# Kernel optimization log

Hardware: AMD Instinct MI355X
Metric: run time of the kernel (lower is better)

The kernel has to match this reference:

```python
import math
import jax, jax.numpy as jnp
import numpy as np

EMB_DIM = 1024
CFG_N_HEADS = 16
# Faithful to the torch module: n_heads collapses to 1 when config.n_heads < emb_dim
N_HEADS = CFG_N_HEADS if CFG_N_HEADS >= EMB_DIM else 1


def setup_inputs() -> dict:
    key = jax.random.key(0)
    ks = jax.random.split(key, 11)
    B, T, C = 4, 2048, EMB_DIM
    s = 1.0 / math.sqrt(C)
    return {
        "q": jax.random.normal(ks[0], (B, T, C), jnp.float32),
        "k": jax.random.normal(ks[1], (B, T, C), jnp.float32),
        "v": jax.random.normal(ks[2], (B, T, C), jnp.float32),
        "Wq": jax.random.normal(ks[3], (C, C), jnp.float32) * s,
        "bq": jax.random.normal(ks[4], (C,), jnp.float32) * s,
        "Wk": jax.random.normal(ks[5], (C, C), jnp.float32) * s,
        "bk": jax.random.normal(ks[6], (C,), jnp.float32) * s,
        "Wv": jax.random.normal(ks[7], (C, C), jnp.float32) * s,
        "bv": jax.random.normal(ks[8], (C,), jnp.float32) * s,
        "Wff": jax.random.normal(ks[9], (C, C), jnp.float32) * s,
        "bff": jax.random.normal(ks[10], (C,), jnp.float32) * s,
    }


def reference(q, k, v, Wq, bq, Wk, bk, Wv, bv, Wff, bff):
    B, T, C = q.shape
    H = N_HEADS
    D = C // H  # head dim (== C here since H degenerates to 1)
    # torch Linear: x @ W.T + b
    qp = (q @ Wq.T + bq).reshape(B, T, H, D).transpose(0, 2, 1, 3)  # [B,H,T,D]
    kp = (k @ Wk.T + bk).reshape(B, T, H, D).transpose(0, 2, 1, 3)
    vp = (v @ Wv.T + bv).reshape(B, T, H, D).transpose(0, 2, 1, 3)
    scale = 1.0 / math.sqrt(D)
    scores = jnp.einsum('bhqd,bhkd->bhqk', qp, kp) * scale  # [B,H,T,T]
    causal = jnp.tril(jnp.ones((T, T), dtype=bool))
    scores = jnp.where(causal[None, None, :, :], scores, -jnp.inf)
    attn = jax.nn.softmax(scores, axis=-1)
    out = jnp.einsum('bhqk,bhkd->bhqd', attn, vp)  # [B,H,T,D]
    out = out.transpose(0, 2, 1, 3).reshape(B, T, C)
    return out @ Wff.T + bff
```

## Files before the change

### kernel.cpp

```cpp
#include <hip/hip_runtime.h>
#include <stdint.h>

typedef unsigned short u16;
typedef short v8s __attribute__((ext_vector_type(8)));
typedef float v4f __attribute__((ext_vector_type(4)));

#define BM 128
#define BN 128
#define BK 64

__device__ __forceinline__ float b2f(u16 b) {
  union { unsigned u; float f; } x; x.u = ((unsigned)b) << 16; return x.f;
}
__device__ __forceinline__ u16 f2b(float f) {
  union { float f; unsigned u; } x; x.f = f;
  unsigned r = x.u + 0x7fffu + ((x.u >> 16) & 1u);
  return (u16)(r >> 16);
}

__device__ __forceinline__ void async_copy16(const void* g, void* lds) {
  __builtin_amdgcn_global_load_lds(
      (const __attribute__((address_space(1))) void*)g,
      (__attribute__((address_space(3))) void*)(uint32_t)(uintptr_t)lds,
      16, 0, 0);
}

__device__ __forceinline__ void xcd_swz(int& bx, int& by) {
  const int gx = gridDim.x;
  const int nwg = gx * gridDim.y;
  const int ord = blockIdx.y * gx + blockIdx.x;
  const int q = nwg >> 3, r = nwg & 7;
  const int xcd = ord & 7, local = ord >> 3;
  const int base = xcd < r ? xcd * (q + 1) : r * (q + 1) + (xcd - r) * q;
  const int s = base + local;
  bx = s % gx;
  by = s / gx;
}

__device__ __forceinline__ void causal_pair_swz(int& bx, int& by) {
  const int gx = gridDim.x;
  const int ord = blockIdx.y * gx + blockIdx.x;
  const int k = ord & 7;
  const int j = ord >> 3;
  by = (j < gx) ? k : 15 - k;
  bx = (j < gx) ? j : j - gx;
}

__global__ __launch_bounds__(256) void cvt3_kernel(
    const float* __restrict__ i0, const float* __restrict__ i1,
    const float* __restrict__ i2, u16* __restrict__ o0, u16* __restrict__ o1,
    u16* __restrict__ o2, int n) {
  const int z = blockIdx.y;
  const float* in = z == 0 ? i0 : (z == 1 ? i1 : i2);
  u16* out = z == 0 ? o0 : (z == 1 ? o1 : o2);
  const int i = (blockIdx.x * 256 + threadIdx.x) * 8;
  if (i >= n) return;
  v4f a = *(const v4f*)(in + i);
  v4f b = *(const v4f*)(in + i + 4);
  v8s o;
#pragma unroll
  for (int j = 0; j < 4; j++) o[j] = (short)f2b(a[j]);
#pragma unroll
  for (int j = 0; j < 4; j++) o[4 + j] = (short)f2b(b[j]);
  *(v8s*)(out + i) = o;
}

__global__ __launch_bounds__(256) void cvt4_kernel(
    const float* __restrict__ i0, const float* __restrict__ i1,
    const float* __restrict__ i2, const float* __restrict__ i3,
    u16* __restrict__ o0, u16* __restrict__ o1, u16* __restrict__ o2,
    u16* __restrict__ o3, int n) {
  const int z = blockIdx.y;
  const float* in = z == 0 ? i0 : (z == 1 ? i1 : (z == 2 ? i2 : i3));
  u16* out = z == 0 ? o0 : (z == 1 ? o1 : (z == 2 ? o2 : o3));
  const int i = (blockIdx.x * 256 + threadIdx.x) * 8;
  if (i >= n) return;
  v4f a = *(const v4f*)(in + i);
  v4f b = *(const v4f*)(in + i + 4);
  v8s o;
#pragma unroll
  for (int j = 0; j < 4; j++) o[j] = (short)f2b(a[j]);
#pragma unroll
  for (int j = 0; j < 4; j++) o[4 + j] = (short)f2b(b[j]);
  *(v8s*)(out + i) = o;
}

template <bool HAS_BIAS, bool CAUSAL_K, bool OUT_F32>
__device__ __forceinline__ void gemm_body(
    const u16* __restrict__ A, int lda, const u16* __restrict__ Bm, int ldb,
    void* __restrict__ Cout_, int ldc, long cbase,
    const float* __restrict__ bias, int K, int m0, int n0) {
  __shared__ u16 ldsA[BM * BK];
  __shared__ u16 ldsB[BN * BK];

  const int tid = threadIdx.x;
  const int wave = tid >> 6, lane = tid & 63;
  const int wm = (wave >> 1) * 64, wn = (wave & 1) * 64;
  const int lrow = lane & 15, quad = lane >> 4;

  v4f acc[4][4];
#pragma unroll
  for (int i = 0; i < 4; i++)
#pragma unroll
    for (int j = 0; j < 4; j++) acc[i][j] = v4f{0.f, 0.f, 0.f, 0.f};

  int Keff = K;
  if (CAUSAL_K) {
    int ke = m0 + BM;
    Keff = ke < K ? ke : K;
  }

  const int rA = lane >> 3;
  const int uch = (lane & 7) ^ rA;
  const u16* pA = A + (long)(m0 + wave * 8 + rA) * lda + uch * 8;
  const u16* pB = Bm + (long)(n0 + wave * 8 + rA) * ldb + uch * 8;
  u16* dA = ldsA + (wave * 8) * BK;
  u16* dB = ldsB + (wave * 8) * BK;

  for (int k0 = 0; k0 < Keff; k0 += BK) {
#pragma unroll
    for (int c = 0; c < 4; c++) {
      async_copy16(pA + (long)c * 32 * lda + k0, dA + c * 32 * BK);
      async_copy16(pB + (long)c * 32 * ldb + k0, dB + c * 32 * BK);
    }
    __syncthreads();

#pragma unroll
    for (int ks = 0; ks < 2; ks++) {
      v8s af[4], bfr[4];
#pragma unroll
      for (int mt = 0; mt < 4; mt++) {
        const int r = wm + mt * 16 + lrow;
        af[mt] =
            *(const v8s*)&ldsA[r * BK + ((ks * 4 + quad) ^ (r & 7)) * 8];
      }
#pragma unroll
      for (int nt = 0; nt < 4; nt++) {
        const int r = wn + nt * 16 + lrow;
        bfr[nt] =
            *(const v8s*)&ldsB[r * BK + ((ks * 4 + quad) ^ (r & 7)) * 8];
      }
#pragma unroll
      for (int mt = 0; mt < 4; mt++)
#pragma unroll
        for (int nt = 0; nt < 4; nt++)
          acc[mt][nt] = __builtin_amdgcn_mfma_f32_16x16x32_bf16(
              af[mt], bfr[nt], acc[mt][nt], 0, 0, 0);
    }
    __syncthreads();
  }

#pragma unroll
  for (int mt = 0; mt < 4; mt++) {
    const int rowBase = m0 + wm + mt * 16 + quad * 4;
#pragma unroll
    for (int nt = 0; nt < 4; nt++) {
      const int col = n0 + wn + nt * 16 + lrow;
      float bv = 0.f;
      if (HAS_BIAS) bv = bias[col];
#pragma unroll
      for (int i = 0; i < 4; i++) {
        const long idx = cbase + (long)(rowBase + i) * ldc + col;
        const float val = acc[mt][nt][i] + bv;
        if (OUT_F32)
          ((float*)Cout_)[idx] = val;
        else
          ((u16*)Cout_)[idx] = f2b(val);
      }
    }
  }
}

__global__ __launch_bounds__(256, 4) void qkv_gemm_kernel(
    const u16* __restrict__ a0, const u16* __restrict__ a1,
    const u16* __restrict__ a2, const u16* __restrict__ w0,
    const u16* __restrict__ w1, const u16* __restrict__ w2,
    const float* __restrict__ b0, const float* __restrict__ b1,
    const float* __restrict__ b2, u16* __restrict__ c0, u16* __restrict__ c1,
    u16* __restrict__ c2, int C) {
  const int z = blockIdx.z;
  const u16* A = z == 0 ? a0 : (z == 1 ? a1 : a2);
  const u16* W = z == 0 ? w0 : (z == 1 ? w1 : w2);
  const float* bias = z == 0 ? b0 : (z == 1 ? b1 : b2);
  u16* Cp = z == 0 ? c0 : (z == 1 ? c1 : c2);
  int bx, by;
  xcd_swz(bx, by);
  gemm_body<true, false, false>(A, C, W, C, Cp, C, 0,
                                bias, C, by * BM, bx * BN);
}

template <bool HAS_BIAS, bool CAUSAL_SKIP, bool CAUSAL_K, bool OUT_F32,
          int SWZ>
__global__ __launch_bounds__(256, 4) void gemm_bt_kernel(
    const u16* __restrict__ A, int lda, long sA,
    const u16* __restrict__ Bm, int ldb, long sB,
    void* __restrict__ Cout_, int ldc, long sC,
    const float* __restrict__ bias, int K) {
  int bx, by;
  if (SWZ == 1)
    causal_pair_swz(bx, by);
  else
    xcd_swz(bx, by);
  const int m0 = by * BM;
  const int n0 = bx * BN;
  if (CAUSAL_SKIP && n0 > m0) return;
  const int z = blockIdx.z;
  gemm_body<HAS_BIAS, CAUSAL_K, OUT_F32>(
      A + (long)z * sA, lda, Bm + (long)z * sB, ldb, Cout_, ldc,
      (long)z * sC, bias, K, m0, n0);
}

__global__ __launch_bounds__(256) void transpose_kernel(
    const u16* __restrict__ in, u16* __restrict__ out) {
  __shared__ u16 tile[64][72];
  const int b = blockIdx.z;
  const int d0 = blockIdx.x * 64;
  const int t0 = blockIdx.y * 64;
  const u16* ip = in + (long)b * 2048 * 1024;
  u16* op = out + (long)b * 1024 * 2048;
  const int tid = threadIdx.x;
  const int tl = tid >> 2;
  const int dl = (tid & 3) * 16;
  const u16* src = ip + (long)(t0 + tl) * 1024 + d0 + dl;
  *(v8s*)&tile[tl][dl] = *(const v8s*)src;
  *(v8s*)&tile[tl][dl + 8] = *(const v8s*)(src + 8);
  __syncthreads();
  const int dd = tid >> 2;
  const int tt = (tid & 3) * 16;
  u16* dst = op + (long)(d0 + dd) * 2048 + t0 + tt;
  v8s o0, o1;
#pragma unroll
  for (int j = 0; j < 8; j++) o0[j] = (short)tile[tt + j][dd];
#pragma unroll
  for (int j = 0; j < 8; j++) o1[j] = (short)tile[tt + 8 + j][dd];
  *(v8s*)dst = o0;
  *(v8s*)(dst + 8) = o1;
}

__global__ __launch_bounds__(256) void softmax_kernel(u16* __restrict__ S) {
  const float scale = 0.03125f;
  const int wave = threadIdx.x >> 6, lane = threadIdx.x & 63;
  const int i = blockIdx.x * 4 + wave, b = blockIdx.y;
  u16* row = S + ((long)b * 2048 + (long)i) * 2048;
  const int Lw = ((i >> 7) + 1) << 7;
  float v[32];
  float m = -1e30f;
#pragma unroll
  for (int c = 0; c < 4; c++) {
    const int jb = c * 512 + lane * 8;
    v8s raw = {0, 0, 0, 0, 0, 0, 0, 0};
    if (jb <= i) raw = *(const v8s*)&row[jb];
#pragma unroll
    for (int jj = 0; jj < 8; jj++) {
      float x = (jb + jj <= i) ? b2f((u16)raw[jj]) * scale : -1e30f;
      v[c * 8 + jj] = x;
      m = fmaxf(m, x);
    }
  }
#pragma unroll
  for (int off = 32; off; off >>= 1) m = fmaxf(m, __shfl_xor(m, off));
  float s = 0.f;
#pragma unroll
  for (int c = 0; c < 4; c++)
#pragma unroll
    for (int jj = 0; jj < 8; jj++) {
      float e = (v[c * 8 + jj] > -1e29f) ? __expf(v[c * 8 + jj] - m) : 0.f;
      v[c * 8 + jj] = e;
      s += e;
    }
#pragma unroll
  for (int off = 32; off; off >>= 1) s += __shfl_xor(s, off);
  const float inv = 1.0f / s;
#pragma unroll
  for (int c = 0; c < 4; c++) {
    const int jb = c * 512 + lane * 8;
    if (jb < Lw) {
      v8s o;
#pragma unroll
      for (int jj = 0; jj < 8; jj++) o[jj] = (short)f2b(v[c * 8 + jj] * inv);
      *(v8s*)&row[jb] = o;
    }
  }
}

extern "C" void kernel_launch(void* const* d_in, const int* in_sizes, int n_in,
                              void* d_out, int out_size, void* d_ws,
                              size_t ws_size, hipStream_t stream) {
  const float* q = (const float*)d_in[0];
  const float* k = (const float*)d_in[1];
  const float* v = (const float*)d_in[2];
  const float* Wq = (const float*)d_in[3];
  const float* bq = (const float*)d_in[4];
  const float* Wk = (const float*)d_in[5];
  const float* bk = (const float*)d_in[6];
  const float* Wv = (const float*)d_in[7];
  const float* bv = (const float*)d_in[8];
  const float* Wff = (const float*)d_in[9];
  const float* bff = (const float*)d_in[10];
  float* out = (float*)d_out;

  const int B = 4, T = 2048, C = 1024, M = B * T;
  const size_t MC = (size_t)M * C;
  const size_t CC = (size_t)C * C;
  u16* ws = (u16*)d_ws;
  u16* qb = ws;
  u16* kb = qb + MC;
  u16* vb = kb + MC;
  u16* Wqb = vb + MC;
  u16* Wkb = Wqb + CC;
  u16* Wvb = Wkb + CC;
  u16* Wffb = Wvb + CC;
  u16* Qp = Wffb + CC;
  u16* Kp = Qp + MC;
  u16* Vp = Kp + MC;
  u16* VpT = Vp + MC;
  u16* S = qb;
  u16* attn = Vp;

  dim3 blk(256);
  cvt3_kernel<<<dim3((int)(MC / 2048), 3), blk, 0, stream>>>(
      q, k, v, qb, kb, vb, (int)MC);
  cvt4_kernel<<<dim3((int)(CC / 2048), 4), blk, 0, stream>>>(
      Wq, Wk, Wv, Wff, Wqb, Wkb, Wvb, Wffb, (int)CC);

  qkv_gemm_kernel<<<dim3(C / BN, M / BM, 3), blk, 0, stream>>>(
      qb, kb, vb, Wqb, Wkb, Wvb, bq, bk, bv, Qp, Kp, Vp, C);
  transpose_kernel<<<dim3(C / 64, T / 64, B), blk, 0, stream>>>(Vp, VpT);
  gemm_bt_kernel<false, true, false, false, 1>
      <<<dim3(T / BN, T / BM, B), blk, 0, stream>>>(
          Qp, C, (long)T * C, Kp, C, (long)T * C, S, T, (long)T * T,
          nullptr, C);
  softmax_kernel<<<dim3(T / 4, B), blk, 0, stream>>>(S);
  gemm_bt_kernel<false, false, true, false, 1>
      <<<dim3(C / BN, T / BM, B), blk, 0, stream>>>(
          S, T, (long)T * T, VpT, T, (long)C * T, attn, C, (long)T * C,
          nullptr, T);
  gemm_bt_kernel<true, false, false, true, 0>
      <<<dim3(C / BN, M / BM, 1), blk, 0, stream>>>(
          attn, C, 0, Wffb, C, 0, out, C, 0, bff, C);
}
```

Before: 327.9 us.

## Fuse V transpose into QKV GEMM epilogue and merge conversion kernels

The V projection GEMM now writes its output transposed, staging the tile through LDS, which removes the separate transpose kernel and its extra global read/write of Vp. The two fp32-to-bf16 conversion launches are merged into a single seven-slice launch to save one kernel launch. The LDS buffer grows slightly for the transpose staging, and the merged conversion grid launches many idle blocks for the smaller weight slices.

```diff
diff --git a/kernel.cpp b/kernel.cpp
--- a/kernel.cpp
+++ b/kernel.cpp
@@ -46,13 +46,26 @@
   bx = (j < gx) ? j : j - gx;
 }
 
-__global__ __launch_bounds__(256) void cvt3_kernel(
+__global__ __launch_bounds__(256) void cvt_all_kernel(
     const float* __restrict__ i0, const float* __restrict__ i1,
-    const float* __restrict__ i2, u16* __restrict__ o0, u16* __restrict__ o1,
-    u16* __restrict__ o2, int n) {
+    const float* __restrict__ i2, const float* __restrict__ i3,
+    const float* __restrict__ i4, const float* __restrict__ i5,
+    const float* __restrict__ i6, u16* __restrict__ o0, u16* __restrict__ o1,
+    u16* __restrict__ o2, u16* __restrict__ o3, u16* __restrict__ o4,
+    u16* __restrict__ o5, u16* __restrict__ o6, int n_big, int n_small) {
   const int z = blockIdx.y;
-  const float* in = z == 0 ? i0 : (z == 1 ? i1 : i2);
-  u16* out = z == 0 ? o0 : (z == 1 ? o1 : o2);
+  const float* in;
+  u16* out;
+  int n;
+  switch (z) {
+    case 0: in = i0; out = o0; n = n_big; break;
+    case 1: in = i1; out = o1; n = n_big; break;
+    case 2: in = i2; out = o2; n = n_big; break;
+    case 3: in = i3; out = o3; n = n_small; break;
+    case 4: in = i4; out = o4; n = n_small; break;
+    case 5: in = i5; out = o5; n = n_small; break;
+    default: in = i6; out = o6; n = n_small; break;
+  }
   const int i = (blockIdx.x * 256 + threadIdx.x) * 8;
   if (i >= n) return;
   v4f a = *(const v4f*)(in + i);
@@ -65,33 +78,19 @@
   *(v8s*)(out + i) = o;
 }
 
-__global__ __launch_bounds__(256) void cvt4_kernel(
-    const float* __restrict__ i0, const float* __restrict__ i1,
-    const float* __restrict__ i2, const float* __restrict__ i3,
-    u16* __restrict__ o0, u16* __restrict__ o1, u16* __restrict__ o2,
-    u16* __restrict__ o3, int n) {
-  const int z = blockIdx.y;
-  const float* in = z == 0 ? i0 : (z == 1 ? i1 : (z == 2 ? i2 : i3));
-  u16* out = z == 0 ? o0 : (z == 1 ? o1 : (z == 2 ? o2 : o3));
-  const int i = (blockIdx.x * 256 + threadIdx.x) * 8;
-  if (i >= n) return;
-  v4f a = *(const v4f*)(in + i);
-  v4f b = *(const v4f*)(in + i + 4);
-  v8s o;
-#pragma unroll
-  for (int j = 0; j < 4; j++) o[j] = (short)f2b(a[j]);
-#pragma unroll
-  for (int j = 0; j < 4; j++) o[4 + j] = (short)f2b(b[j]);
-  *(v8s*)(out + i) = o;
-}
-
-template <bool HAS_BIAS, bool CAUSAL_K, bool OUT_F32>
+union LdsU {
+  struct { u16 a[BM * BK]; u16 b[BN * BK]; } s;
+  u16 t[128 * 136];
+};
+
+template <bool HAS_BIAS, bool CAUSAL_K, bool OUT_F32, bool TR_OUT>
 __device__ __forceinline__ void gemm_body(
     const u16* __restrict__ A, int lda, const u16* __restrict__ Bm, int ldb,
     void* __restrict__ Cout_, int ldc, long cbase,
     const float* __restrict__ bias, int K, int m0, int n0) {
-  __shared__ u16 ldsA[BM * BK];
-  __shared__ u16 ldsB[BN * BK];
+  __shared__ LdsU lds;
+  u16* ldsA = lds.s.a;
+  u16* ldsB = lds.s.b;
 
   const int tid = threadIdx.x;
   const int wave = tid >> 6, lane = tid & 63;
@@ -148,6 +147,32 @@
               af[mt], bfr[nt], acc[mt][nt], 0, 0, 0);
     }
     __syncthreads();
+  }
+
+  if (TR_OUT) {
+#pragma unroll
+    for (int mt = 0; mt < 4; mt++) {
+      const int rl = wm + mt * 16 + quad * 4;
+#pragma unroll
+      for (int nt = 0; nt < 4; nt++) {
+        const int cl = wn + nt * 16 + lrow;
+        float bv = 0.f;
+        if (HAS_BIAS) bv = bias[n0 + cl];
+#pragma unroll
+        for (int i = 0; i < 4; i++)
+          lds.t[cl * 136 + rl + i] = f2b(acc[mt][nt][i] + bv);
+      }
+    }
+    __syncthreads();
+    const int cl2 = tid >> 1, th = (tid & 1) * 64;
+    const long bbase =
+        (long)(m0 >> 11) * ((long)1024 * 2048) + (long)(m0 & 2047);
+    u16* dst = (u16*)Cout_ + bbase + (long)(n0 + cl2) * 2048 + th;
+    const u16* srcl = &lds.t[cl2 * 136 + th];
+#pragma unroll
+    for (int j = 0; j < 8; j++)
+      *(v8s*)(dst + j * 8) = *(const v8s*)(srcl + j * 8);
+    return;
   }
 
 #pragma unroll
@@ -185,8 +210,12 @@
   u16* Cp = z == 0 ? c0 : (z == 1 ? c1 : c2);
   int bx, by;
   xcd_swz(bx, by);
-  gemm_body<true, false, false>(A, C, W, C, Cp, C, 0,
-                                bias, C, by * BM, bx * BN);
+  if (z == 2)
+    gemm_body<true, false, false, true>(A, C, W, C, Cp, C, 0, bias, C,
+                                        by * BM, bx * BN);
+  else
+    gemm_body<true, false, false, false>(A, C, W, C, Cp, C, 0, bias, C,
+                                         by * BM, bx * BN);
 }
 
 template <bool HAS_BIAS, bool CAUSAL_SKIP, bool CAUSAL_K, bool OUT_F32,
@@ -205,36 +234,9 @@
   const int n0 = bx * BN;
   if (CAUSAL_SKIP && n0 > m0) return;
   const int z = blockIdx.z;
-  gemm_body<HAS_BIAS, CAUSAL_K, OUT_F32>(
+  gemm_body<HAS_BIAS, CAUSAL_K, OUT_F32, false>(
       A + (long)z * sA, lda, Bm + (long)z * sB, ldb, Cout_, ldc,
       (long)z * sC, bias, K, m0, n0);
-}
-
-__global__ __launch_bounds__(256) void transpose_kernel(
-    const u16* __restrict__ in, u16* __restrict__ out) {
-  __shared__ u16 tile[64][72];
-  const int b = blockIdx.z;
-  const int d0 = blockIdx.x * 64;
-  const int t0 = blockIdx.y * 64;
-  const u16* ip = in + (long)b * 2048 * 1024;
-  u16* op = out + (long)b * 1024 * 2048;
-  const int tid = threadIdx.x;
-  const int tl = tid >> 2;
-  const int dl = (tid & 3) * 16;
-  const u16* src = ip + (long)(t0 + tl) * 1024 + d0 + dl;
-  *(v8s*)&tile[tl][dl] = *(const v8s*)src;
-  *(v8s*)&tile[tl][dl + 8] = *(const v8s*)(src + 8);
-  __syncthreads();
-  const int dd = tid >> 2;
-  const int tt = (tid & 3) * 16;
-  u16* dst = op + (long)(d0 + dd) * 2048 + t0 + tt;
-  v8s o0, o1;
-#pragma unroll
-  for (int j = 0; j < 8; j++) o0[j] = (short)tile[tt + j][dd];
-#pragma unroll
-  for (int j = 0; j < 8; j++) o1[j] = (short)tile[tt + 8 + j][dd];
-  *(v8s*)dst = o0;
-  *(v8s*)(dst + 8) = o1;
 }
 
 __global__ __launch_bounds__(256) void softmax_kernel(u16* __restrict__ S) {
@@ -318,14 +320,12 @@
   u16* attn = Vp;
 
   dim3 blk(256);
-  cvt3_kernel<<<dim3((int)(MC / 2048), 3), blk, 0, stream>>>(
-      q, k, v, qb, kb, vb, (int)MC);
-  cvt4_kernel<<<dim3((int)(CC / 2048), 4), blk, 0, stream>>>(
-      Wq, Wk, Wv, Wff, Wqb, Wkb, Wvb, Wffb, (int)CC);
+  cvt_all_kernel<<<dim3((int)(MC / 2048), 7), blk, 0, stream>>>(
+      q, k, v, Wq, Wk, Wv, Wff, qb, kb, vb, Wqb, Wkb, Wvb, Wffb,
+      (int)MC, (int)CC);
 
   qkv_gemm_kernel<<<dim3(C / BN, M / BM, 3), blk, 0, stream>>>(
-      qb, kb, vb, Wqb, Wkb, Wvb, bq, bk, bv, Qp, Kp, Vp, C);
-  transpose_kernel<<<dim3(C / 64, T / 64, B), blk, 0, stream>>>(Vp, VpT);
+      qb, kb, vb, Wqb, Wkb, Wvb, bq, bk, bv, Qp, Kp, VpT, C);
   gemm_bt_kernel<false, true, false, false, 1>
       <<<dim3(T / BN, T / BM, B), blk, 0, stream>>>(
           Qp, C, (long)T * C, Kp, C, (long)T * C, S, T, (long)T * T,
```

Result: no change. 332.4 us (+1.4%).
